# Kernel optimization log

Hardware: AMD Instinct MI355X
Metric: run time of the kernel (lower is better)

Reference implementation:

```python
import jax, jax.numpy as jnp
import numpy as np

NUM_HEADS = 16
HEAD_DIM = 128
RMS_EPS = 1e-6


def _rms_norm(x):
    # RMSNorm over last dim, no learned weight
    return x * jax.lax.rsqrt(jnp.mean(jnp.square(x), axis=-1, keepdims=True) + RMS_EPS)


def _rotary_cos_sin(T, head_dim, dtype=jnp.float32):
    # half-truncated RoPE: quarter of dims get frequencies, next quarter gets freq 0
    dim_quarter = max(1, head_dim // 4)
    angular_freq = (1.0 / 1024.0) ** jnp.linspace(0.0, 1.0, dim_quarter, dtype=dtype)
    angular_freq = jnp.concatenate([angular_freq, jnp.zeros(dim_quarter, dtype=dtype)])  # [head_dim//2]
    t = jnp.arange(T, dtype=dtype)
    theta = t[:, None] * angular_freq[None, :]  # [T, head_dim//2]
    return jnp.cos(theta), jnp.sin(theta)


def _apply_rotary(x_BTHD, cos, sin):
    # x: [B,T,H,D]; cos/sin: [T, D//2]
    c = cos[None, :, None, :]
    s = sin[None, :, None, :]
    x1, x2 = jnp.split(x_BTHD, 2, axis=-1)
    y1 = x1 * c + x2 * s
    y2 = -x1 * s + x2 * c
    return jnp.concatenate([y1, y2], axis=-1)


def setup_inputs() -> dict:
    key = jax.random.key(0)
    k1, k2, k3 = jax.random.split(key, 3)
    B, T, dim = 1, 2048, 2048
    hdim = NUM_HEADS * HEAD_DIM
    std = 0.5 * dim ** (-0.5)
    x = jax.random.normal(k1, (B, T, dim), dtype=jnp.float32)
    Wqkv = jax.random.normal(k2, (3, hdim, dim), dtype=jnp.float32) * std
    Wout = jax.random.normal(k3, (dim, hdim), dtype=jnp.float32) * std
    return {"x": x, "Wqkv": Wqkv, "Wout": Wout}


def reference(x, Wqkv, Wout):
    B, T, dim = x.shape
    H, D = NUM_HEADS, HEAD_DIM
    scale = 1.0 / (D ** 0.5)

    # fused QKV projection: [B,T,3,H,D]
    qkv = jnp.einsum('btd,ehd->bteh'.replace('eh', 'f'), x, Wqkv.reshape(3 * H * D, dim))  # [B,T,3HD]
    qkv = qkv.reshape(B, T, 3, H, D)
    q, k, v = qkv[:, :, 0], qkv[:, :, 1], qkv[:, :, 2]  # each [B,T,H,D]

    q, k = _rms_norm(q), _rms_norm(k)
    cos, sin = _rotary_cos_sin(T, D, dtype=jnp.float32)
    q, k = _apply_rotary(q, cos, sin), _apply_rotary(k, cos, sin)

    # causal attention
    scores = jnp.einsum('bthd,bshd->bhts', q, k) * scale  # [B,H,T,T]
    causal = jnp.tril(jnp.ones((T, T), dtype=bool))
    scores = jnp.where(causal[None, None], scores, -jnp.inf)
    probs = jax.nn.softmax(scores, axis=-1)
    y = jnp.einsum('bhts,bshd->bthd', probs, v)  # [B,T,H,D]

    y = y.reshape(B, T, H * D)
    return y @ Wout.T
```

## Files before the change

kernel.cpp:

```cpp
#include <hip/hip_runtime.h>
#include <hip/hip_bf16.h>
#include <stdint.h>

typedef __hip_bfloat16 bf16;
typedef __bf16 bf16x8 __attribute__((ext_vector_type(8)));
typedef float f32x4 __attribute__((ext_vector_type(4)));

#define MFMA16(a, b, c) __builtin_amdgcn_mfma_f32_16x16x32_bf16((a), (b), (c), 0, 0, 0)

__device__ __forceinline__ void gload_lds16(const void* g, void* l) {
    __builtin_amdgcn_global_load_lds((const __attribute__((address_space(1))) void*)g,
                                     (__attribute__((address_space(3))) void*)l, 16, 0, 0);
}

struct alignas(16) B8 { bf16 v[8]; };
struct alignas(8)  B4 { bf16 v[4]; };

__global__ __launch_bounds__(256) void cast_all_k(
    const float* __restrict__ x, const float* __restrict__ wqkv, const float* __restrict__ wout,
    bf16* __restrict__ xb, bf16* __restrict__ wqkvb, bf16* __restrict__ woutb) {
    const size_t NX = (size_t)2048 * 2048 / 8;
    const size_t NW = (size_t)3 * 2048 * 2048 / 8;
    size_t i = (size_t)blockIdx.x * 256 + threadIdx.x;
    const float* s; bf16* d;
    if (i < NX)            { s = x;    d = xb; }
    else if (i < NX + NW)  { s = wqkv; d = wqkvb; i -= NX; }
    else                   { s = wout; d = woutb; i -= NX + NW; }
    float4 a = ((const float4*)s)[2 * i];
    float4 b = ((const float4*)s)[2 * i + 1];
    B8 t;
    t.v[0] = __float2bfloat16(a.x); t.v[1] = __float2bfloat16(a.y);
    t.v[2] = __float2bfloat16(a.z); t.v[3] = __float2bfloat16(a.w);
    t.v[4] = __float2bfloat16(b.x); t.v[5] = __float2bfloat16(b.y);
    t.v[6] = __float2bfloat16(b.z); t.v[7] = __float2bfloat16(b.w);
    ((B8*)d)[i] = t;
}

__global__ __launch_bounds__(256) void gemm_bt(
    const bf16* __restrict__ A, const bf16* __restrict__ B, float* __restrict__ C,
    int M, int N, int K) {
    __shared__ __align__(16) bf16 As[2][128 * 32];
    __shared__ __align__(16) bf16 Bs[2][128 * 32];
    const int t = threadIdx.x;
    const int lane = t & 63, w = t >> 6;
    const int wr = w >> 1, wc = w & 1;
    const int l15 = lane & 15, lg = lane >> 4;
    const int m0 = blockIdx.y * 128, n0 = blockIdx.x * 128;

    const int row = t >> 2, cb = t & 3;
    const int row1 = (t + 256) >> 2, cb1 = t & 3;

    f32x4 acc[4][4] = {};

#define G_STAGE(buf, k0)                                                        \
    do {                                                                        \
        gload_lds16(&A[(size_t)(m0 + row) * K + (k0) + cb * 8],                 \
                    &As[buf][t * 8]);                                           \
        gload_lds16(&B[(size_t)(n0 + row) * K + (k0) + cb * 8],                 \
                    &Bs[buf][t * 8]);                                           \
        gload_lds16(&A[(size_t)(m0 + row1) * K + (k0) + cb1 * 8],               \
                    &As[buf][(t + 256) * 8]);                                   \
        gload_lds16(&B[(size_t)(n0 + row1) * K + (k0) + cb1 * 8],               \
                    &Bs[buf][(t + 256) * 8]);                                   \
    } while (0)

    G_STAGE(0, 0);
    int cur = 0;
    for (int k0 = 0; k0 < K; k0 += 32) {
        const bool hn = (k0 + 32 < K);
        if (hn) {
            G_STAGE(cur ^ 1, k0 + 32);
            asm volatile("s_waitcnt vmcnt(4)" ::: "memory");
        } else {
            asm volatile("s_waitcnt vmcnt(0)" ::: "memory");
        }
        __builtin_amdgcn_s_barrier();
        __builtin_amdgcn_sched_barrier(0);

        bf16x8 af[4], bfr[4];
#pragma unroll
        for (int mi = 0; mi < 4; ++mi)
            af[mi] = *(const bf16x8*)&As[cur][(wr * 64 + mi * 16 + l15) * 32 + lg * 8];
#pragma unroll
        for (int ni = 0; ni < 4; ++ni)
            bfr[ni] = *(const bf16x8*)&Bs[cur][(wc * 64 + ni * 16 + l15) * 32 + lg * 8];
#pragma unroll
        for (int mi = 0; mi < 4; ++mi)
#pragma unroll
            for (int ni = 0; ni < 4; ++ni)
                acc[mi][ni] = MFMA16(af[mi], bfr[ni], acc[mi][ni]);
        __builtin_amdgcn_s_barrier();
        cur ^= 1;
    }
#undef G_STAGE

#pragma unroll
    for (int mi = 0; mi < 4; ++mi) {
        int r0 = m0 + wr * 64 + mi * 16 + lg * 4;
#pragma unroll
        for (int ni = 0; ni < 4; ++ni) {
            int c0 = n0 + wc * 64 + ni * 16 + l15;
#pragma unroll
            for (int j = 0; j < 4; ++j)
                C[(size_t)(r0 + j) * N + c0] = acc[mi][ni][j];
        }
    }
}

__global__ __launch_bounds__(128) void normrope_k(
    const float* __restrict__ qkv, bf16* __restrict__ qb, bf16* __restrict__ kb) {
    const int t = blockIdx.x, h = blockIdx.y, d = threadIdx.x;
    const float* base = qkv + (size_t)t * 6144;
    float q = base[h * 128 + d];
    float k = base[2048 + h * 128 + d];

    __shared__ float red[4];
    __shared__ float qn[128], kn[128];
    float sq = q * q, sk = k * k;
#pragma unroll
    for (int m = 1; m <= 32; m <<= 1) {
        sq += __shfl_xor(sq, m);
        sk += __shfl_xor(sk, m);
    }
    if ((d & 63) == 0) { red[(d >> 6) * 2] = sq; red[(d >> 6) * 2 + 1] = sk; }
    __syncthreads();
    float rq = rsqrtf((red[0] + red[2]) * (1.0f / 128.0f) + 1e-6f);
    float rk = rsqrtf((red[1] + red[3]) * (1.0f / 128.0f) + 1e-6f);
    qn[d] = q * rq;
    kn[d] = k * rk;
    __syncthreads();

    int j = d & 63;
    float c = 1.0f, s = 0.0f;
    if (j < 32) {
        float af = exp2f(-10.0f * (float)j / 31.0f);
        float theta = (float)t * af;
        sincosf(theta, &s, &c);
    }
    float oq, ok;
    if (d < 64) { oq =  qn[d] * c + qn[d + 64] * s;  ok =  kn[d] * c + kn[d + 64] * s; }
    else        { oq = -qn[d - 64] * s + qn[d] * c;  ok = -kn[d - 64] * s + kn[d] * c; }

    size_t oidx = ((size_t)h * 2048 + t) * 128 + d;
    qb[oidx] = __float2bfloat16(oq * 0.08838834764831845f);
    kb[oidx] = __float2bfloat16(ok);
}

__global__ __launch_bounds__(256) void vtrans_k(
    const float* __restrict__ qkv, bf16* __restrict__ vt) {
    __shared__ bf16 Ts[64][72];
    const int t0 = blockIdx.x * 64, d0 = blockIdx.y * 64, h = blockIdx.z;
    const int tid = threadIdx.x;
#pragma unroll
    for (int it = 0; it < 4; ++it) {
        int f = tid + it * 256;
        int tl = f >> 4, dl = (f & 15) * 4;
        float4 v = *(const float4*)&qkv[(size_t)(t0 + tl) * 6144 + 4096 + h * 128 + d0 + dl];
        Ts[tl][dl + 0] = __float2bfloat16(v.x);
        Ts[tl][dl + 1] = __float2bfloat16(v.y);
        Ts[tl][dl + 2] = __float2bfloat16(v.z);
        Ts[tl][dl + 3] = __float2bfloat16(v.w);
    }
    __syncthreads();
#pragma unroll
    for (int it = 0; it < 2; ++it) {
        int f = tid + it * 256;
        int dl = f >> 3, tc = f & 7;
        B8 p;
#pragma unroll
        for (int i = 0; i < 8; ++i) p.v[i] = Ts[tc * 8 + i][dl];
        *(B8*)&vt[((size_t)h * 128 + d0 + dl) * 2048 + t0 + tc * 8] = p;
    }
}

__global__ __launch_bounds__(256) void attn_main_k(
    const bf16* __restrict__ qg, const bf16* __restrict__ kg,
    const bf16* __restrict__ vt, char* __restrict__ part) {
    const int T = 2048, D = 128;
    const int cz = blockIdx.x, qt = blockIdx.y, h = blockIdx.z;
    if (cz > (qt >> 2)) return;
    const int qb0 = qt * 64;
    const int kstart = cz * 256;
    const int kend = min(kstart + 256, (qt + 1) * 64);

    __shared__ __align__(16) bf16 Ks[64 * 128];
    __shared__ __align__(16) bf16 Vs[128 * 64];
    __shared__ __align__(16) bf16 Ps[4][16 * 64];

    const int t = threadIdx.x;
    const int lane = t & 63, w = t >> 6;
    const int l15 = lane & 15, lg = lane >> 4;

    const size_t qoff = ((size_t)h * T + qb0 + w * 16 + l15) * D;
    bf16x8 qf[4];
#pragma unroll
    for (int ks = 0; ks < 4; ++ks)
        qf[ks] = *(const bf16x8*)&qg[qoff + ks * 32 + lg * 8];

    bf16x8 onesf;
#pragma unroll
    for (int i = 0; i < 8; ++i) onesf[i] = (__bf16)1.0f;

    f32x4 o[8] = {};
    float mrow[4] = {-1e30f, -1e30f, -1e30f, -1e30f};
    float lrow[4] = {0.f, 0.f, 0.f, 0.f};

    for (int k0 = kstart; k0 < kend; k0 += 64) {
#pragma unroll
        for (int c = 0; c < 4; ++c) {
            int f = t + c * 256;
            int krow = f >> 4, kc = f & 15;
            gload_lds16(&kg[((size_t)h * T + k0 + krow) * D + ((kc ^ (krow & 15)) * 8)],
                        &Ks[f * 8]);
            int dr = f >> 3, vc = f & 7;
            gload_lds16(&vt[((size_t)h * D + dr) * T + k0 + ((vc ^ (dr & 7)) * 8)],
                        &Vs[f * 8]);
        }
        __syncthreads();

        f32x4 sc[4] = {};
#pragma unroll
        for (int ks = 0; ks < 4; ++ks) {
#pragma unroll
            for (int nb = 0; nb < 4; ++nb) {
                int key = nb * 16 + l15;
                int c = ks * 4 + lg;
                bf16x8 kf = *(const bf16x8*)&Ks[key * 128 + ((c ^ (key & 15)) * 8)];
                sc[nb] = MFMA16(qf[ks], kf, sc[nb]);
            }
        }

        const bool diag = (k0 == qb0);
        const int qrow_base = qb0 + w * 16 + lg * 4;
        float fac[4];
        bool anyresc = false;
#pragma unroll
        for (int j = 0; j < 4; ++j) {
            float s0 = sc[0][j], s1 = sc[1][j], s2 = sc[2][j], s3 = sc[3][j];
            if (diag) {
                int qrow = qrow_base + j;
                if (k0 + l15 > qrow)      s0 = -1e30f;
                if (k0 + 16 + l15 > qrow) s1 = -1e30f;
                if (k0 + 32 + l15 > qrow) s2 = -1e30f;
                if (k0 + 48 + l15 > qrow) s3 = -1e30f;
            }
            float tm = fmaxf(fmaxf(s0, s1), fmaxf(s2, s3));
            tm = fmaxf(tm, __shfl_xor(tm, 1));
            tm = fmaxf(tm, __shfl_xor(tm, 2));
            tm = fmaxf(tm, __shfl_xor(tm, 4));
            tm = fmaxf(tm, __shfl_xor(tm, 8));
            if (__all(tm <= mrow[j] + 6.0f)) {
                fac[j] = 1.0f;
            } else {
                float mnew = fmaxf(mrow[j], tm);
                fac[j] = __expf(mrow[j] - mnew);
                mrow[j] = mnew;
                anyresc = true;
            }
            float p0 = __expf(s0 - mrow[j]), p1 = __expf(s1 - mrow[j]);
            float p2 = __expf(s2 - mrow[j]), p3 = __expf(s3 - mrow[j]);
            int prow = lg * 4 + j;
            int sub = l15 & 7, hi = l15 >> 3;
            bf16* pw = &Ps[w][prow * 64 + sub];
            pw[(((0 + hi) ^ (prow & 7)) * 8)] = __float2bfloat16(p0);
            pw[(((2 + hi) ^ (prow & 7)) * 8)] = __float2bfloat16(p1);
            pw[(((4 + hi) ^ (prow & 7)) * 8)] = __float2bfloat16(p2);
            pw[(((6 + hi) ^ (prow & 7)) * 8)] = __float2bfloat16(p3);
        }

        if (anyresc) {
#pragma unroll
            for (int nd = 0; nd < 8; ++nd)
#pragma unroll
                for (int j = 0; j < 4; ++j) o[nd][j] *= fac[j];
        }

        f32x4 lsum = {};
#pragma unroll
        for (int hk = 0; hk < 2; ++hk) {
            bf16x8 pf = *(const bf16x8*)&Ps[w][l15 * 64 + (((hk * 4 + lg) ^ (l15 & 7)) * 8)];
            lsum = MFMA16(pf, onesf, lsum);
#pragma unroll
            for (int nd = 0; nd < 8; ++nd) {
                int dd = nd * 16 + l15;
                bf16x8 vf = *(const bf16x8*)&Vs[dd * 64 + (((hk * 4 + lg) ^ (dd & 7)) * 8)];
                o[nd] = MFMA16(pf, vf, o[nd]);
            }
        }
#pragma unroll
        for (int j = 0; j < 4; ++j) lrow[j] = lrow[j] * fac[j] + lsum[j];
        __syncthreads();
    }

    int B = qt >> 2, r4 = qt & 3;
    int slot = h * 144 + qt + 2 * B * (B - 1) + r4 * B + cz;
    char* rec = part + (size_t)slot * 16896;
    float* mrec = (float*)rec;
    float* lrec = (float*)(rec + 256);
    bf16*  orec = (bf16*)(rec + 512);
    if (l15 == 0) {
#pragma unroll
        for (int j = 0; j < 4; ++j) {
            mrec[w * 16 + lg * 4 + j] = mrow[j];
            lrec[w * 16 + lg * 4 + j] = lrow[j];
        }
    }
#pragma unroll
    for (int nd = 0; nd < 8; ++nd)
#pragma unroll
        for (int j = 0; j < 4; ++j)
            orec[(w * 16 + lg * 4 + j) * 128 + nd * 16 + l15] = __float2bfloat16(o[nd][j]);
}

__global__ __launch_bounds__(256) void attn_merge_k(
    const char* __restrict__ part, bf16* __restrict__ y) {
    const int qt = blockIdx.x, h = blockIdx.y, tid = threadIdx.x;
    const int nch = (qt >> 2) + 1;
    int B = qt >> 2, r4 = qt & 3;
    const int base = h * 144 + qt + 2 * B * (B - 1) + r4 * B;
    const int r = tid >> 2;
    const int d0 = (tid & 3) * 32;

    float mi[8], li[8], wgt[8];
    float M = -1e30f;
#pragma unroll
    for (int i = 0; i < 8; ++i) {
        if (i < nch) {
            const char* rec = part + (size_t)(base + i) * 16896;
            mi[i] = ((const float*)rec)[r];
            li[i] = ((const float*)(rec + 256))[r];
            M = fmaxf(M, mi[i]);
        } else { mi[i] = -1e30f; li[i] = 0.f; }
    }
    float L = 0.f;
#pragma unroll
    for (int i = 0; i < 8; ++i) {
        wgt[i] = (i < nch) ? __expf(mi[i] - M) : 0.f;
        L += li[i] * wgt[i];
    }
    float invL = 1.0f / L;

    bf16* yrow = &y[(size_t)(qt * 64 + r) * 2048 + h * 128 + d0];
#pragma unroll
    for (int dd = 0; dd < 32; dd += 8) {
        float facc[8] = {};
#pragma unroll
        for (int i = 0; i < 8; ++i) {
            if (i < nch) {
                const bf16* orec = (const bf16*)(part + (size_t)(base + i) * 16896 + 512);
                B8 ov = *(const B8*)&orec[r * 128 + d0 + dd];
#pragma unroll
                for (int e = 0; e < 8; ++e)
                    facc[e] += wgt[i] * __bfloat162float(ov.v[e]);
            }
        }
        B8 p;
#pragma unroll
        for (int e = 0; e < 8; ++e) p.v[e] = __float2bfloat16(facc[e] * invL);
        *(B8*)&yrow[dd] = p;
    }
}

extern "C" void kernel_launch(void* const* d_in, const int* in_sizes, int n_in,
                              void* d_out, int out_size, void* d_ws, size_t ws_size,
                              hipStream_t stream) {
    const float* x    = (const float*)d_in[0];
    const float* wqkv = (const float*)d_in[1];
    const float* wout = (const float*)d_in[2];
    float* out = (float*)d_out;

    char* ws = (char*)d_ws;
    bf16*  xb    = (bf16*)(ws);
    bf16*  wqkvb = (bf16*)(ws + 8388608);
    bf16*  woutb = (bf16*)(ws + 33554432);
    float* qkvf  = (float*)(ws + 41943040);
    bf16*  qb    = (bf16*)(ws + 92274688);
    bf16*  kb    = (bf16*)(ws + 100663296);
    bf16*  vt    = (bf16*)(ws + 109051904);
    bf16*  yb    = (bf16*)(ws + 117440512);

    cast_all_k<<<10240, 256, 0, stream>>>(x, wqkv, wout, xb, wqkvb, woutb);
    gemm_bt<<<dim3(48, 16), 256, 0, stream>>>(xb, wqkvb, qkvf, 2048, 6144, 2048);
    normrope_k<<<dim3(2048, 16), 128, 0, stream>>>(qkvf, qb, kb);
    vtrans_k<<<dim3(32, 2, 16), 256, 0, stream>>>(qkvf, vt);
    attn_main_k<<<dim3(8, 32, 16), 256, 0, stream>>>(qb, kb, vt, (char*)qkvf);
    attn_merge_k<<<dim3(32, 16), 256, 0, stream>>>((const char*)qkvf, yb);
    gemm_bt<<<dim3(16, 16), 256, 0, stream>>>(yb, woutb, out, 2048, 2048, 2048);
}
```

Before: 355.7 us.

## Replace QKV projection GEMM with 256x192-tile kernel using swizzled LDS

Adds a dedicated QKV GEMM kernel with 512 threads, 256x192 output tiles, and K-step 64. It uses XOR-swizzled shared-memory layout to avoid bank conflicts and a grid swizzle that maps 256 blocks onto the 8x32 tile grid. The larger tiles raise arithmetic intensity and cut global/LDS traffic relative to the old 128x128 kernel. The cost is heavy LDS use (~112KB) and many accumulator registers, which limit occupancy. The tile count exactly matches 256 CUs, one block each.

Measured after the change: 354.6 us. No clear change (-0.3%).

```diff
diff --git a/kernel.cpp b/kernel.cpp
--- a/kernel.cpp
+++ b/kernel.cpp
@@ -36,6 +36,91 @@
     ((B8*)d)[i] = t;
 }
 
+__global__ __launch_bounds__(512, 2) void gemm256_bt(
+    const bf16* __restrict__ A, const bf16* __restrict__ B, float* __restrict__ C) {
+    const int K = 2048, N = 6144;
+    __shared__ __align__(16) bf16 As[2][256 * 64];
+    __shared__ __align__(16) bf16 Bs[2][192 * 64];
+
+    const int t = threadIdx.x;
+    const int lane = t & 63, w = t >> 6;
+    const int wm = w >> 2, wn = w & 3;
+    const int l15 = lane & 15, lg = lane >> 4;
+
+    const int bid = blockIdx.x;
+    const int swz = (bid & 7) * 32 + (bid >> 3);
+    const int m0 = (swz >> 5) * 256;
+    const int n0 = (swz & 31) * 192;
+
+    f32x4 acc[8][3] = {};
+
+#define S256(buf, k0)                                                            \
+    do {                                                                         \
+        _Pragma("unroll")                                                        \
+        for (int i = 0; i < 4; ++i) {                                            \
+            int f = t + i * 512;                                                 \
+            int r = f >> 3, c = f & 7;                                           \
+            gload_lds16(&A[(size_t)(m0 + r) * K + (k0) + ((c ^ (r & 7)) * 8)],   \
+                        &As[buf][f * 8]);                                        \
+        }                                                                        \
+        _Pragma("unroll")                                                        \
+        for (int i = 0; i < 3; ++i) {                                            \
+            int f = t + i * 512;                                                 \
+            int r = f >> 3, c = f & 7;                                           \
+            gload_lds16(&B[(size_t)(n0 + r) * K + (k0) + ((c ^ (r & 7)) * 8)],   \
+                        &Bs[buf][f * 8]);                                        \
+        }                                                                        \
+    } while (0)
+
+    S256(0, 0);
+    int cur = 0;
+    for (int k0 = 0; k0 < K; k0 += 64) {
+        if (k0 + 64 < K) {
+            S256(cur ^ 1, k0 + 64);
+            asm volatile("s_waitcnt vmcnt(7)" ::: "memory");
+        } else {
+            asm volatile("s_waitcnt vmcnt(0)" ::: "memory");
+        }
+        __builtin_amdgcn_s_barrier();
+        __builtin_amdgcn_sched_barrier(0);
+
+#pragma unroll
+        for (int kk = 0; kk < 2; ++kk) {
+            bf16x8 bfr[3];
+#pragma unroll
+            for (int ni = 0; ni < 3; ++ni) {
+                int row = wn * 48 + ni * 16 + l15;
+                int c = (kk * 4 + lg) ^ (row & 7);
+                bfr[ni] = *(const bf16x8*)&Bs[cur][row * 64 + c * 8];
+            }
+#pragma unroll
+            for (int mi = 0; mi < 8; ++mi) {
+                int row = wm * 128 + mi * 16 + l15;
+                int c = (kk * 4 + lg) ^ (row & 7);
+                bf16x8 af = *(const bf16x8*)&As[cur][row * 64 + c * 8];
+#pragma unroll
+                for (int ni = 0; ni < 3; ++ni)
+                    acc[mi][ni] = MFMA16(af, bfr[ni], acc[mi][ni]);
+            }
+        }
+        __builtin_amdgcn_s_barrier();
+        cur ^= 1;
+    }
+#undef S256
+
+#pragma unroll
+    for (int mi = 0; mi < 8; ++mi) {
+        int r0 = m0 + wm * 128 + mi * 16 + lg * 4;
+#pragma unroll
+        for (int ni = 0; ni < 3; ++ni) {
+            int c0 = n0 + wn * 48 + ni * 16 + l15;
+#pragma unroll
+            for (int j = 0; j < 4; ++j)
+                C[(size_t)(r0 + j) * N + c0] = acc[mi][ni][j];
+        }
+    }
+}
+
 __global__ __launch_bounds__(256) void gemm_bt(
     const bf16* __restrict__ A, const bf16* __restrict__ B, float* __restrict__ C,
     int M, int N, int K) {
@@ -380,7 +465,7 @@
     bf16*  yb    = (bf16*)(ws + 117440512);
 
     cast_all_k<<<10240, 256, 0, stream>>>(x, wqkv, wout, xb, wqkvb, woutb);
-    gemm_bt<<<dim3(48, 16), 256, 0, stream>>>(xb, wqkvb, qkvf, 2048, 6144, 2048);
+    gemm256_bt<<<256, 512, 0, stream>>>(xb, wqkvb, qkvf);
     normrope_k<<<dim3(2048, 16), 128, 0, stream>>>(qkvf, qb, kb);
     vtrans_k<<<dim3(32, 2, 16), 256, 0, stream>>>(qkvf, vt);
     attn_main_k<<<dim3(8, 32, 16), 256, 0, stream>>>(qb, kb, vt, (char*)qkvf);
```
